# Optimization experiments

Measured on AMD Instinct MI355X. Metric: run time of the kernel, lower is better.

The kernel has to match this reference:

```python
import jax, jax.numpy as jnp
import numpy as np

SIZE = 512
ATTN = 64      # per-head attention_size
OUT = 64       # per-head output_size
HEADS = 8

def setup_inputs() -> dict:
    key = jax.random.key(0)
    ks = jax.random.split(key, 7)
    s = 0.02
    return {
        "x":  jax.random.normal(ks[0], (4, 2048, SIZE), dtype=jnp.float32),
        "Wq": jax.random.normal(ks[1], (SIZE, ATTN * HEADS), dtype=jnp.float32) * s,
        "bq": jax.random.normal(ks[2], (ATTN * HEADS,), dtype=jnp.float32) * s,
        "Wk": jax.random.normal(ks[3], (SIZE, ATTN), dtype=jnp.float32) * s,  # shared key, no bias
        "Wv": jax.random.normal(ks[4], (SIZE, OUT * HEADS), dtype=jnp.float32) * s,
        "bv": jax.random.normal(ks[5], (OUT * HEADS,), dtype=jnp.float32) * s,
    }

def reference(x, Wq, bq, Wk, Wv, bv):
    B, S, _ = x.shape
    q = (x @ Wq + bq).reshape(B, S, HEADS, ATTN)   # (B,S,H,A)
    k = x @ Wk                                      # (B,S,A) shared across heads
    v = (x @ Wv + bv).reshape(B, S, HEADS, OUT)     # (B,S,H,O)
    # NOTE: original divides by sqrt(seq_len), not sqrt(head_dim)
    scale = 1.0 / np.sqrt(S).astype(np.float32)
    scores = jnp.einsum("bqha,bka->bhqk", q, k) * scale  # (B,H,S,S)
    causal = jnp.tril(jnp.ones((S, S), dtype=bool))
    scores = jnp.where(causal, scores, -jnp.inf)
    attn = jax.nn.softmax(scores, axis=-1)
    out = jnp.einsum("bhqk,bkho->bqho", attn, v)    # (B,S,H,O)
    return out.reshape(B, S, HEADS * OUT)
```

## Files before the change

kernel.cpp:

```cpp
#include <hip/hip_runtime.h>
#include <math.h>


typedef _Float16 half8 __attribute__((ext_vector_type(8)));
typedef _Float16 half4 __attribute__((ext_vector_type(4)));
typedef float float4v __attribute__((ext_vector_type(4)));
typedef unsigned int u32;

#define SCL2E 0.031885926f

__device__ inline float4v mfma16(half8 a, half8 b, float4v c) {
    return __builtin_amdgcn_mfma_f32_16x16x32_f16(a, b, c, 0, 0, 0);
}
__device__ inline void load16(const _Float16* g, _Float16* l) {
    __builtin_amdgcn_global_load_lds((const __attribute__((address_space(1))) u32*)g,
                                     (__attribute__((address_space(3))) u32*)l, 16, 0, 0);
}

__global__ __launch_bounds__(256) void prep(
    const float* __restrict__ x, const float* __restrict__ Wq,
    const float* __restrict__ Wk, const float* __restrict__ Wv,
    _Float16* __restrict__ xh, _Float16* __restrict__ wqt,
    _Float16* __restrict__ wkt, _Float16* __restrict__ wvt) {
    const int bid = blockIdx.x;
    if (bid < 2048) {
        size_t base = (size_t)bid * 2048 + (size_t)threadIdx.x * 8;
        const float4* xp = (const float4*)(x + base);
        float4 f0 = xp[0], f1 = xp[1];
        half8 h = {(_Float16)f0.x, (_Float16)f0.y, (_Float16)f0.z, (_Float16)f0.w,
                   (_Float16)f1.x, (_Float16)f1.y, (_Float16)f1.z, (_Float16)f1.w};
        *(half8*)(xh + base) = h;
    } else {
        int r = bid - 2048;
        const float* W; _Float16* WT; int N, bx, by;
        if (r < 256)      { W = Wq; WT = wqt; N = 512; bx = r & 15; by = r >> 4; }
        else if (r < 288) { r -= 256; W = Wk; WT = wkt; N = 64;  bx = r & 1;  by = r >> 1; }
        else              { r -= 288; W = Wv; WT = wvt; N = 512; bx = r & 15; by = r >> 4; }
        __shared__ float T[32][33];
        const int tx = threadIdx.x & 31, ty = threadIdx.x >> 5;
        const int n0 = bx * 32, k0 = by * 32;
#pragma unroll
        for (int i = 0; i < 4; ++i)
            T[ty + 8 * i][tx] = W[(size_t)(k0 + ty + 8 * i) * N + n0 + tx];
        __syncthreads();
#pragma unroll
        for (int i = 0; i < 4; ++i)
            WT[(size_t)(n0 + ty + 8 * i) * 512 + k0 + tx] = (_Float16)T[tx][ty + 8 * i];
    }
}

__global__ __launch_bounds__(256) void qkv_gemm(
    const _Float16* __restrict__ xh,
    const _Float16* __restrict__ wqt, const _Float16* __restrict__ wkt,
    const _Float16* __restrict__ wvt,
    const float* __restrict__ bq, const float* __restrict__ bv,
    _Float16* __restrict__ q_ws, _Float16* __restrict__ kt_ws, _Float16* __restrict__ vt_ws) {
    __shared__ __align__(16) _Float16 Xs[8192];
    __shared__ __align__(16) _Float16 Ws[4096];

    const int m0 = blockIdx.x * 128;
    const int nt = blockIdx.y;
    const _Float16* WT;
    const float* bias;
    if (nt < 8)       { WT = wqt + (size_t)nt * 64 * 512; bias = bq + nt * 64; }
    else if (nt == 8) { WT = wkt;                          bias = nullptr; }
    else              { WT = wvt + (size_t)(nt - 9) * 64 * 512; bias = bv + (nt - 9) * 64; }

    const int tid = threadIdx.x;
    const int w = tid >> 6, lane = tid & 63, quad = lane >> 4, cl = lane & 15;
    const int lrow = lane >> 3;
    const int lgc = (lane & 7) ^ lrow;
    const _Float16* xg = xh + (size_t)(m0 + lrow) * 512 + lgc * 8;
    const _Float16* wg = WT + (size_t)lrow * 512 + lgc * 8;

    const int g0 = (quad ^ (cl & 7)) << 3;
    const int g1 = ((quad ^ 4) ^ (cl & 7)) << 3;

    float4v acc[2][4] = {};

    for (int ki = 0; ki < 8; ++ki) {
        const int kk = ki * 64;
        __syncthreads();
#pragma unroll
        for (int c = 0; c < 4; ++c) {
            int cc = w * 4 + c;
            load16(xg + (size_t)cc * 8 * 512 + kk, Xs + cc * 512);
        }
#pragma unroll
        for (int c = 0; c < 2; ++c) {
            int cc = w * 2 + c;
            load16(wg + (size_t)cc * 8 * 512 + kk, Ws + cc * 512);
        }
        __syncthreads();
#pragma unroll
        for (int c = 0; c < 2; ++c) {
            const int g = c ? g1 : g0;
#pragma unroll
            for (int s = 0; s < 2; ++s) {
                half8 a = *(const half8*)(Xs + (w * 32 + s * 16 + cl) * 64 + g);
#pragma unroll
                for (int j = 0; j < 4; ++j) {
                    half8 b = *(const half8*)(Ws + (j * 16 + cl) * 64 + g);
                    acc[s][j] = mfma16(a, b, acc[s][j]);
                }
            }
        }
    }

    if (nt < 8) {
#pragma unroll
        for (int s = 0; s < 2; ++s)
#pragma unroll
            for (int j = 0; j < 4; ++j)
#pragma unroll
                for (int r = 0; r < 4; ++r) {
                    int lr = w * 32 + s * 16 + quad * 4 + r;
                    int col = j * 16 + cl;
                    q_ws[(size_t)(m0 + lr) * 512 + nt * 64 + col] =
                        (_Float16)((acc[s][j][r] + bias[col]) * SCL2E);
                }
    } else if (nt == 8) {
#pragma unroll
        for (int s = 0; s < 2; ++s)
#pragma unroll
            for (int j = 0; j < 4; ++j)
#pragma unroll
                for (int r = 0; r < 4; ++r) {
                    int grow = m0 + w * 32 + s * 16 + quad * 4 + r;
                    int b = grow >> 11, t = (grow >> 6) & 31, row = grow & 63;
                    int col = j * 16 + cl;
                    kt_ws[((size_t)(b * 32 + t) << 12) + row * 64 +
                          (((col >> 3) ^ (row & 7)) << 3) + (col & 7)] = (_Float16)acc[s][j][r];
                }
    } else {
        const int h = nt - 9;
#pragma unroll
        for (int s = 0; s < 2; ++s)
#pragma unroll
            for (int j = 0; j < 4; ++j)
#pragma unroll
                for (int r = 0; r < 4; ++r) {
                    int grow = m0 + w * 32 + s * 16 + quad * 4 + r;
                    int b = grow >> 11, t = (grow >> 6) & 31, row = grow & 63;
                    int o = j * 16 + cl;
                    int kap = ((row & 15) << 2) + (row >> 4);
                    vt_ws[(((size_t)(b * 8 + h) * 32 + t) << 12) + o * 64 +
                          (((kap >> 3) ^ (o & 7)) << 3) + (kap & 7)] =
                        (_Float16)(acc[s][j][r] + bias[o]);
                }
    }
}

__global__ __launch_bounds__(512) void attn(
    const _Float16* __restrict__ q_ws, const _Float16* __restrict__ kt_ws,
    const _Float16* __restrict__ vt_ws, float* __restrict__ out) {
    __shared__ __align__(16) _Float16 Ks[2][4096];
    __shared__ __align__(16) _Float16 VTs[2][4096];
    __shared__ __align__(16) _Float16 Ps[8][1024];

    const int bh = blockIdx.x, b = bh >> 3, h = bh & 7;
    const int pair = blockIdx.y;
    const int bS = b * 2048;
    const int tid = threadIdx.x;
    const int w = tid >> 6, lane = tid & 63, quad = lane >> 4, cl = lane & 15;

    const _Float16* kbase = kt_ws + ((size_t)(b * 32) << 12);
    const _Float16* vbase = vt_ws + ((size_t)((b * 8 + h) * 32) << 12);

    const int g0 = (quad ^ (cl & 7)) << 3;
    const int g1 = ((quad ^ 4) ^ (cl & 7)) << 3;
    const int soff = w * 512 + lane * 8;

    for (int phase = 0; phase < 2; ++phase) {
        const int qt = phase ? (15 - pair) : pair;
        const int tlast = 2 * qt + 1;
        const int q0 = qt * 128;

        const _Float16* qbase = q_ws + (size_t)(bS + q0 + w * 16 + cl) * 512 + h * 64;
        half8 qa0 = *(const half8*)(qbase + quad * 8);
        half8 qa1 = *(const half8*)(qbase + 32 + quad * 8);

        float4v oacc[4] = {};
        float l_run[4] = {0.f, 0.f, 0.f, 0.f};

        __syncthreads();
        load16(kbase + soff, &Ks[0][soff]);
        load16(vbase + soff, &VTs[0][soff]);

        for (int t = 0; t <= tlast; ++t) {
            __syncthreads();
            if (t < tlast) {
                const size_t off = (size_t)(t + 1) << 12;
                const int nb = (t + 1) & 1;
                load16(kbase + off + soff, &Ks[nb][soff]);
                load16(vbase + off + soff, &VTs[nb][soff]);
            }
            const int bb = t & 1;
            const int ww = (t == tlast) ? (w - 4) : ((t == 2 * qt) ? w : 100);
            if (ww >= 0) {
                const int jmax = ww < 3 ? ww : 3;
                float4v sfr[4];
#pragma unroll
                for (int j = 0; j < 4; ++j) {
                    if (j <= jmax) {
                        const _Float16* kr = &Ks[bb][(j * 16 + cl) * 64];
                        half8 b0 = *(const half8*)(kr + g0);
                        half8 b1 = *(const half8*)(kr + g1);
                        float4v a_ = {0.f, 0.f, 0.f, 0.f};
                        a_ = mfma16(qa0, b0, a_);
                        a_ = mfma16(qa1, b1, a_);
                        sfr[j] = a_;
                    }
                }
#pragma unroll
                for (int r = 0; r < 4; ++r) {
                    float pj[4];
#pragma unroll
                    for (int j = 0; j < 4; ++j) {
                        bool live = (j < jmax) ||
                                    (j == jmax && (ww > 3 || cl <= quad * 4 + r));
                        pj[j] = live ? exp2f(sfr[j][r]) : 0.f;
                    }
                    l_run[r] += (pj[0] + pj[1]) + (pj[2] + pj[3]);
                    int rr = quad * 4 + r;
                    half4 ph = {(_Float16)pj[0], (_Float16)pj[1], (_Float16)pj[2], (_Float16)pj[3]};
                    *(half4*)&Ps[w][rr * 64 + ((((cl >> 1) ^ (rr & 7)) << 3) | ((cl & 1) << 2))] = ph;
                }
                const _Float16* PB = &Ps[w][cl * 64];
                half8 pa0 = *(const half8*)(PB + g0);
                half8 pa1 = *(const half8*)(PB + g1);
#pragma unroll
                for (int jo = 0; jo < 4; ++jo) {
                    const _Float16* vr = &VTs[bb][(jo * 16 + cl) * 64];
                    half8 v0 = *(const half8*)(vr + g0);
                    half8 v1 = *(const half8*)(vr + g1);
                    oacc[jo] = mfma16(pa0, v0, oacc[jo]);
                    oacc[jo] = mfma16(pa1, v1, oacc[jo]);
                }
            }
        }
#pragma unroll
        for (int r = 0; r < 4; ++r) {
            float l = l_run[r];
            l += __shfl_xor(l, 1);
            l += __shfl_xor(l, 2);
            l += __shfl_xor(l, 4);
            l += __shfl_xor(l, 8);
            float inv = 1.0f / l;
            int row = q0 + w * 16 + quad * 4 + r;
            float* op = out + (size_t)(bS + row) * 512 + h * 64 + cl;
            op[0]  = oacc[0][r] * inv;
            op[16] = oacc[1][r] * inv;
            op[32] = oacc[2][r] * inv;
            op[48] = oacc[3][r] * inv;
        }
    }
}

extern "C" void kernel_launch(void* const* d_in, const int* in_sizes, int n_in,
                              void* d_out, int out_size, void* d_ws, size_t ws_size,
                              hipStream_t stream) {
    const float* x  = (const float*)d_in[0];
    const float* Wq = (const float*)d_in[1];
    const float* bq = (const float*)d_in[2];
    const float* Wk = (const float*)d_in[3];
    const float* Wv = (const float*)d_in[4];
    const float* bv = (const float*)d_in[5];
    float* out = (float*)d_out;

    char* ws = (char*)d_ws;
    _Float16* q_ws  = (_Float16*)(ws);
    _Float16* kt_ws = (_Float16*)(ws + 8388608);
    _Float16* vt_ws = (_Float16*)(ws + 9437184);
    _Float16* wqt   = (_Float16*)(ws + 17825792);
    _Float16* wkt   = (_Float16*)(ws + 18350080);
    _Float16* wvt   = (_Float16*)(ws + 18415616);
    _Float16* xh    = (_Float16*)(ws + 18939904);

    prep<<<dim3(2592), dim3(256), 0, stream>>>(x, Wq, Wk, Wv, xh, wqt, wkt, wvt);

    qkv_gemm<<<dim3(64, 17), dim3(256), 0, stream>>>(
        xh, wqt, wkt, wvt, bq, bv, q_ws, kt_ws, vt_ws);

    attn<<<dim3(32, 8), dim3(512), 0, stream>>>(q_ws, kt_ws, vt_ws, out);
}
```

Baseline: 152.5 us.

## Stage GEMM epilogue through LDS and give each attention wave two query tiles

The QKV GEMM epilogue now writes results into shared memory in the target swizzled layout, then copies them to global memory with coalesced 16-byte stores instead of scattered 2-byte stores. The attention kernel drops to 256 threads, with each wave handling 32 query rows (two 16-row sub-tiles). This lets each K/V fragment loaded from LDS be reused across both sub-tiles and separates unmasked tiles into a fast path. The trade-off is fewer waves per block and higher register pressure, which could lower occupancy and latency hiding.

```diff
diff --git a/kernel.cpp b/kernel.cpp
--- a/kernel.cpp
+++ b/kernel.cpp
@@ -55,8 +55,10 @@
     const _Float16* __restrict__ wvt,
     const float* __restrict__ bq, const float* __restrict__ bv,
     _Float16* __restrict__ q_ws, _Float16* __restrict__ kt_ws, _Float16* __restrict__ vt_ws) {
-    __shared__ __align__(16) _Float16 Xs[8192];
-    __shared__ __align__(16) _Float16 Ws[4096];
+    __shared__ __align__(16) _Float16 SB[12288];
+    _Float16* Xs = SB;
+    _Float16* Ws = SB + 8192;
+    _Float16* Cs = SB;
 
     const int m0 = blockIdx.x * 128;
     const int nt = blockIdx.y;
@@ -107,6 +109,7 @@
         }
     }
 
+    __syncthreads();
     if (nt < 8) {
 #pragma unroll
         for (int s = 0; s < 2; ++s)
@@ -114,10 +117,9 @@
             for (int j = 0; j < 4; ++j)
 #pragma unroll
                 for (int r = 0; r < 4; ++r) {
-                    int lr = w * 32 + s * 16 + quad * 4 + r;
+                    int row = w * 32 + s * 16 + quad * 4 + r;
                     int col = j * 16 + cl;
-                    q_ws[(size_t)(m0 + lr) * 512 + nt * 64 + col] =
-                        (_Float16)((acc[s][j][r] + bias[col]) * SCL2E);
+                    Cs[row * 64 + col] = (_Float16)((acc[s][j][r] + bias[col]) * SCL2E);
                 }
     } else if (nt == 8) {
 #pragma unroll
@@ -126,37 +128,57 @@
             for (int j = 0; j < 4; ++j)
 #pragma unroll
                 for (int r = 0; r < 4; ++r) {
-                    int grow = m0 + w * 32 + s * 16 + quad * 4 + r;
-                    int b = grow >> 11, t = (grow >> 6) & 31, row = grow & 63;
+                    int row = w * 32 + s * 16 + quad * 4 + r;
                     int col = j * 16 + cl;
-                    kt_ws[((size_t)(b * 32 + t) << 12) + row * 64 +
-                          (((col >> 3) ^ (row & 7)) << 3) + (col & 7)] = (_Float16)acc[s][j][r];
+                    Cs[row * 64 + ((((col >> 3) ^ (row & 7)) << 3) | (col & 7))] =
+                        (_Float16)acc[s][j][r];
                 }
     } else {
-        const int h = nt - 9;
 #pragma unroll
         for (int s = 0; s < 2; ++s)
 #pragma unroll
             for (int j = 0; j < 4; ++j)
 #pragma unroll
                 for (int r = 0; r < 4; ++r) {
-                    int grow = m0 + w * 32 + s * 16 + quad * 4 + r;
-                    int b = grow >> 11, t = (grow >> 6) & 31, row = grow & 63;
+                    int row = w * 32 + s * 16 + quad * 4 + r;
                     int o = j * 16 + cl;
-                    int kap = ((row & 15) << 2) + (row >> 4);
-                    vt_ws[(((size_t)(b * 8 + h) * 32 + t) << 12) + o * 64 +
-                          (((kap >> 3) ^ (o & 7)) << 3) + (kap & 7)] =
+                    int kap = ((row & 15) << 2) + ((row >> 4) & 3);
+                    Cs[(row >> 6) * 4096 + o * 64 + ((((kap >> 3) ^ (o & 7)) << 3) | (kap & 7))] =
                         (_Float16)(acc[s][j][r] + bias[o]);
                 }
     }
-}
-
-__global__ __launch_bounds__(512) void attn(
+    __syncthreads();
+    const int b = m0 >> 11, t0 = (m0 >> 6) & 31;
+    if (nt < 8) {
+#pragma unroll
+        for (int p = 0; p < 4; ++p) {
+            int idx = p * 2048 + tid * 8;
+            int row = idx >> 6, col = idx & 63;
+            *(half8*)(q_ws + (size_t)(m0 + row) * 512 + nt * 64 + col) = *(const half8*)(Cs + idx);
+        }
+    } else if (nt == 8) {
+        _Float16* ob = kt_ws + ((size_t)(b * 32 + t0) << 12);
+#pragma unroll
+        for (int p = 0; p < 4; ++p) {
+            int idx = p * 2048 + tid * 8;
+            *(half8*)(ob + idx) = *(const half8*)(Cs + idx);
+        }
+    } else {
+        _Float16* ob = vt_ws + (((size_t)(b * 8 + (nt - 9)) * 32 + t0) << 12);
+#pragma unroll
+        for (int p = 0; p < 4; ++p) {
+            int idx = p * 2048 + tid * 8;
+            *(half8*)(ob + idx) = *(const half8*)(Cs + idx);
+        }
+    }
+}
+
+__global__ __launch_bounds__(256) void attn(
     const _Float16* __restrict__ q_ws, const _Float16* __restrict__ kt_ws,
     const _Float16* __restrict__ vt_ws, float* __restrict__ out) {
     __shared__ __align__(16) _Float16 Ks[2][4096];
     __shared__ __align__(16) _Float16 VTs[2][4096];
-    __shared__ __align__(16) _Float16 Ps[8][1024];
+    __shared__ __align__(16) _Float16 Ps[4][2048];
 
     const int bh = blockIdx.x, b = bh >> 3, h = bh & 7;
     const int pair = blockIdx.y;
@@ -169,91 +191,135 @@
 
     const int g0 = (quad ^ (cl & 7)) << 3;
     const int g1 = ((quad ^ 4) ^ (cl & 7)) << 3;
-    const int soff = w * 512 + lane * 8;
+    const int soff = w * 1024 + lane * 8;
+    const int psw = (((cl >> 1)) << 3) | ((cl & 1) << 2);
 
     for (int phase = 0; phase < 2; ++phase) {
         const int qt = phase ? (15 - pair) : pair;
         const int tlast = 2 * qt + 1;
         const int q0 = qt * 128;
 
-        const _Float16* qbase = q_ws + (size_t)(bS + q0 + w * 16 + cl) * 512 + h * 64;
-        half8 qa0 = *(const half8*)(qbase + quad * 8);
-        half8 qa1 = *(const half8*)(qbase + 32 + quad * 8);
-
-        float4v oacc[4] = {};
-        float l_run[4] = {0.f, 0.f, 0.f, 0.f};
+        const _Float16* qb0 = q_ws + (size_t)(bS + q0 + w * 32 + cl) * 512 + h * 64;
+        const _Float16* qb1 = qb0 + 16 * 512;
+        half8 qa[2][2];
+        qa[0][0] = *(const half8*)(qb0 + quad * 8);
+        qa[0][1] = *(const half8*)(qb0 + 32 + quad * 8);
+        qa[1][0] = *(const half8*)(qb1 + quad * 8);
+        qa[1][1] = *(const half8*)(qb1 + 32 + quad * 8);
+
+        float4v oacc[2][4] = {};
+        float l_run[2][4] = {};
 
         __syncthreads();
-        load16(kbase + soff, &Ks[0][soff]);
-        load16(vbase + soff, &VTs[0][soff]);
+        load16(kbase + soff,       &Ks[0][soff]);
+        load16(kbase + soff + 512, &Ks[0][soff + 512]);
+        load16(vbase + soff,       &VTs[0][soff]);
+        load16(vbase + soff + 512, &VTs[0][soff + 512]);
 
         for (int t = 0; t <= tlast; ++t) {
             __syncthreads();
             if (t < tlast) {
                 const size_t off = (size_t)(t + 1) << 12;
                 const int nb = (t + 1) & 1;
-                load16(kbase + off + soff, &Ks[nb][soff]);
-                load16(vbase + off + soff, &VTs[nb][soff]);
+                load16(kbase + off + soff,       &Ks[nb][soff]);
+                load16(kbase + off + soff + 512, &Ks[nb][soff + 512]);
+                load16(vbase + off + soff,       &VTs[nb][soff]);
+                load16(vbase + off + soff + 512, &VTs[nb][soff + 512]);
             }
             const int bb = t & 1;
-            const int ww = (t == tlast) ? (w - 4) : ((t == 2 * qt) ? w : 100);
-            if (ww >= 0) {
-                const int jmax = ww < 3 ? ww : 3;
-                float4v sfr[4];
-#pragma unroll
-                for (int j = 0; j < 4; ++j) {
-                    if (j <= jmax) {
-                        const _Float16* kr = &Ks[bb][(j * 16 + cl) * 64];
-                        half8 b0 = *(const half8*)(kr + g0);
-                        half8 b1 = *(const half8*)(kr + g1);
+            const bool fullt = (t != 2 * qt) && (t != tlast);
+            const int ww0 = fullt ? 100 : (2 * w + (t == tlast ? -4 : 0));
+            const int ww1 = fullt ? 100 : (ww0 + 1);
+            if (ww1 < 0) continue;
+
+            const int jm0 = (ww0 < 3) ? ww0 : 3;
+            const int jm1 = (ww1 < 3) ? ww1 : 3;
+
+            float4v sfr[2][4];
+            if (!fullt) {
+#pragma unroll
+                for (int s = 0; s < 2; ++s)
+#pragma unroll
+                    for (int j = 0; j < 4; ++j) sfr[s][j] = float4v{0.f, 0.f, 0.f, 0.f};
+            }
+#pragma unroll
+            for (int j = 0; j < 4; ++j) {
+                if (j <= jm1) {
+                    const _Float16* kr = &Ks[bb][(j * 16 + cl) * 64];
+                    half8 b0 = *(const half8*)(kr + g0);
+                    half8 b1 = *(const half8*)(kr + g1);
+                    if (j <= jm0) {
                         float4v a_ = {0.f, 0.f, 0.f, 0.f};
-                        a_ = mfma16(qa0, b0, a_);
-                        a_ = mfma16(qa1, b1, a_);
-                        sfr[j] = a_;
+                        a_ = mfma16(qa[0][0], b0, a_);
+                        a_ = mfma16(qa[0][1], b1, a_);
+                        sfr[0][j] = a_;
                     }
-                }
+                    float4v a_ = {0.f, 0.f, 0.f, 0.f};
+                    a_ = mfma16(qa[1][0], b0, a_);
+                    a_ = mfma16(qa[1][1], b1, a_);
+                    sfr[1][j] = a_;
+                }
+            }
+#pragma unroll
+            for (int s = 0; s < 2; ++s) {
+                const int wws = s ? ww1 : ww0;
+                const int jms = s ? jm1 : jm0;
+                const bool nomask = fullt || (wws > 3);
 #pragma unroll
                 for (int r = 0; r < 4; ++r) {
                     float pj[4];
-#pragma unroll
-                    for (int j = 0; j < 4; ++j) {
-                        bool live = (j < jmax) ||
-                                    (j == jmax && (ww > 3 || cl <= quad * 4 + r));
-                        pj[j] = live ? exp2f(sfr[j][r]) : 0.f;
+                    if (nomask) {
+#pragma unroll
+                        for (int j = 0; j < 4; ++j) pj[j] = exp2f(sfr[s][j][r]);
+                    } else {
+#pragma unroll
+                        for (int j = 0; j < 4; ++j) {
+                            bool lv = (j < jms) || (j == jms && cl <= quad * 4 + r);
+                            pj[j] = lv ? exp2f(sfr[s][j][r]) : 0.f;
+                        }
                     }
-                    l_run[r] += (pj[0] + pj[1]) + (pj[2] + pj[3]);
+                    l_run[s][r] += (pj[0] + pj[1]) + (pj[2] + pj[3]);
                     int rr = quad * 4 + r;
                     half4 ph = {(_Float16)pj[0], (_Float16)pj[1], (_Float16)pj[2], (_Float16)pj[3]};
-                    *(half4*)&Ps[w][rr * 64 + ((((cl >> 1) ^ (rr & 7)) << 3) | ((cl & 1) << 2))] = ph;
-                }
-                const _Float16* PB = &Ps[w][cl * 64];
-                half8 pa0 = *(const half8*)(PB + g0);
-                half8 pa1 = *(const half8*)(PB + g1);
-#pragma unroll
-                for (int jo = 0; jo < 4; ++jo) {
-                    const _Float16* vr = &VTs[bb][(jo * 16 + cl) * 64];
-                    half8 v0 = *(const half8*)(vr + g0);
-                    half8 v1 = *(const half8*)(vr + g1);
-                    oacc[jo] = mfma16(pa0, v0, oacc[jo]);
-                    oacc[jo] = mfma16(pa1, v1, oacc[jo]);
-                }
-            }
-        }
-#pragma unroll
-        for (int r = 0; r < 4; ++r) {
-            float l = l_run[r];
-            l += __shfl_xor(l, 1);
-            l += __shfl_xor(l, 2);
-            l += __shfl_xor(l, 4);
-            l += __shfl_xor(l, 8);
-            float inv = 1.0f / l;
-            int row = q0 + w * 16 + quad * 4 + r;
-            float* op = out + (size_t)(bS + row) * 512 + h * 64 + cl;
-            op[0]  = oacc[0][r] * inv;
-            op[16] = oacc[1][r] * inv;
-            op[32] = oacc[2][r] * inv;
-            op[48] = oacc[3][r] * inv;
-        }
+                    *(half4*)&Ps[w][s * 1024 + rr * 64 + (psw ^ ((rr & 7) << 3))] = ph;
+                }
+            }
+            half8 pa[2][2];
+#pragma unroll
+            for (int s = 0; s < 2; ++s) {
+                const _Float16* PB = &Ps[w][s * 1024 + cl * 64];
+                pa[s][0] = *(const half8*)(PB + g0);
+                pa[s][1] = *(const half8*)(PB + g1);
+            }
+#pragma unroll
+            for (int jo = 0; jo < 4; ++jo) {
+                const _Float16* vr = &VTs[bb][(jo * 16 + cl) * 64];
+                half8 v0 = *(const half8*)(vr + g0);
+                half8 v1 = *(const half8*)(vr + g1);
+#pragma unroll
+                for (int s = 0; s < 2; ++s) {
+                    oacc[s][jo] = mfma16(pa[s][0], v0, oacc[s][jo]);
+                    oacc[s][jo] = mfma16(pa[s][1], v1, oacc[s][jo]);
+                }
+            }
+        }
+#pragma unroll
+        for (int s = 0; s < 2; ++s)
+#pragma unroll
+            for (int r = 0; r < 4; ++r) {
+                float l = l_run[s][r];
+                l += __shfl_xor(l, 1);
+                l += __shfl_xor(l, 2);
+                l += __shfl_xor(l, 4);
+                l += __shfl_xor(l, 8);
+                float inv = 1.0f / l;
+                int row = q0 + w * 32 + s * 16 + quad * 4 + r;
+                float* op = out + (size_t)(bS + row) * 512 + h * 64 + cl;
+                op[0]  = oacc[s][0][r] * inv;
+                op[16] = oacc[s][1][r] * inv;
+                op[32] = oacc[s][2][r] * inv;
+                op[48] = oacc[s][3][r] * inv;
+            }
     }
 }
 
@@ -282,5 +348,5 @@
     qkv_gemm<<<dim3(64, 17), dim3(256), 0, stream>>>(
         xh, wqt, wkt, wvt, bq, bv, q_ws, kt_ws, vt_ws);
 
-    attn<<<dim3(32, 8), dim3(512), 0, stream>>>(q_ws, kt_ws, vt_ws, out);
-}
+    attn<<<dim3(32, 8), dim3(256), 0, stream>>>(q_ws, kt_ws, vt_ws, out);
+}
```

After: 165.0 us. +8.2%, slower.
